# Optimization experiments

Hardware: AMD Instinct MI355X
Metric: run time of the kernel (lower is better)

Reference implementation:

```python
import jax, jax.numpy as jnp
import numpy as np


def fps(xyz, npoint):
    # farthest point sampling, starts at index 0 (matches pointnet2 CUDA kernel)
    B, N, _ = xyz.shape
    def step(carry, _):
        min_d, last = carry
        last_xyz = jnp.take_along_axis(xyz, last[:, None, None], axis=1)  # [B,1,3]
        d = jnp.sum((xyz - last_xyz) ** 2, axis=-1)                        # [B,N]
        min_d = jnp.minimum(min_d, d)
        nxt = jnp.argmax(min_d, axis=1).astype(jnp.int32)
        return (min_d, nxt), last
    init = (jnp.full((B, N), 1e10, xyz.dtype), jnp.zeros((B,), jnp.int32))
    _, idx = jax.lax.scan(step, init, None, length=npoint)
    return jnp.transpose(idx)  # [B, npoint]


def ball_query(xyz, new_xyz, radius, nsample):
    # first nsample points within radius; pad with first hit (0 if none) -- CUDA semantics
    N = xyz.shape[1]
    d2 = jnp.sum((new_xyz[:, :, None, :] - xyz[:, None, :, :]) ** 2, axis=-1)  # [B,S,N]
    cand = jnp.where(d2 < radius * radius, jnp.arange(N, dtype=jnp.int32)[None, None, :], N)
    srt = jnp.sort(cand, axis=-1)[..., :nsample]
    first = srt[..., :1]
    first = jnp.where(first == N, 0, first)
    return jnp.where(srt == N, first, srt)  # [B,S,K]


def gather_nbrs(x, idx):
    # x [B,N,C], idx [B,S,K] -> [B,S,K,C]
    B, S, K = idx.shape
    flat = jnp.take_along_axis(x, idx.reshape(B, S * K, 1), axis=1)
    return flat.reshape(B, S, K, x.shape[-1])


def shared_mlp(x, layers):
    # 1x1 conv (+ folded eval-mode BN) + ReLU per layer
    for w, b in layers:
        x = jax.nn.relu(jnp.einsum('bskc,oc->bsko', x, w) + b)
    return x


def sa_module(xyz, feat, npoint, radius, nsample, layers):
    idx = fps(xyz, npoint)
    new_xyz = jnp.take_along_axis(xyz, idx[:, :, None], axis=1)  # [B,S,3]
    gidx = ball_query(xyz, new_xyz, radius, nsample)
    grouped = gather_nbrs(xyz, gidx) - new_xyz[:, :, None, :]    # centered local xyz
    if feat is not None:
        grouped = jnp.concatenate([grouped, gather_nbrs(feat, gidx)], axis=-1)
    x = shared_mlp(grouped, layers)
    return new_xyz, jnp.max(x, axis=2)  # max-pool over neighbors -> [B,S,Cout]


def sa_module_all(xyz, feat, layers):
    # GroupAll: concat raw (uncentered) xyz with features, one group of all points
    x = jnp.concatenate([xyz, feat], axis=-1)[:, None]  # [B,1,N,3+C]
    x = shared_mlp(x, layers)
    return jnp.max(x, axis=2)[:, 0]  # [B,Cout]


def _forward(data, ws):
    B, T, N, _ = data.shape
    xyz = data.reshape(B * T, N, 3)
    xyz, feat = sa_module(xyz, None, 256, 0.2, 32, ws[0])
    xyz, feat = sa_module(xyz, feat, 128, 0.4, 32, ws[1])
    out = sa_module_all(xyz, feat, ws[2])
    return out.reshape(B, T, -1)


DIMS = [(3, 64), (64, 64), (64, 128), (131, 128), (128, 128), (128, 256), (259, 256), (256, 512), (512, 1024)]
NAMES = ['1_0', '1_1', '1_2', '2_0', '2_1', '2_2', '3_0', '3_1', '3_2']


def setup_inputs() -> dict:
    key = jax.random.key(0)
    keys = jax.random.split(key, 1 + 2 * len(DIMS))
    inp = {'data': jax.random.normal(keys[0], (4, 8, 4096, 3), jnp.float32)}
    for i, ((cin, cout), nm) in enumerate(zip(DIMS, NAMES)):
        inp['w' + nm] = jax.random.normal(keys[1 + 2 * i], (cout, cin), jnp.float32) / np.sqrt(cin).astype(np.float32)
        inp['b' + nm] = jax.random.normal(keys[2 + 2 * i], (cout,), jnp.float32) * 0.02
    return inp


def reference(data, w1_0, b1_0, w1_1, b1_1, w1_2, b1_2,
              w2_0, b2_0, w2_1, b2_1, w2_2, b2_2,
              w3_0, b3_0, w3_1, b3_1, w3_2, b3_2):
    ws = [[(w1_0, b1_0), (w1_1, b1_1), (w1_2, b1_2)],
          [(w2_0, b2_0), (w2_1, b2_1), (w2_2, b2_2)],
          [(w3_0, b3_0), (w3_1, b3_1), (w3_2, b3_2)]]
    return _forward(data, ws)
```

## Files before the change

### kernel.cpp

```cpp
#include <hip/hip_runtime.h>
#include <hip/hip_bf16.h>
#include <cstdint>
#include <cstddef>

#define BT 32
#define N1 4096
#define S1 256
#define S2 128
#define KNB 32

typedef __attribute__((ext_vector_type(8))) short short8;
typedef __attribute__((ext_vector_type(4))) float f32x4;

__device__ __forceinline__ float sqdist(float ax, float ay, float az,
                                        float bx, float by, float bz) {
    float dx = __fsub_rn(ax, bx), dy = __fsub_rn(ay, by), dz = __fsub_rn(az, bz);
    return __fadd_rn(__fadd_rn(__fmul_rn(dx, dx), __fmul_rn(dy, dy)), __fmul_rn(dz, dz));
}

__device__ __forceinline__ unsigned short f2bf(float f) {
    unsigned u = __float_as_uint(f);
    return (unsigned short)((u + 0x7FFFu + ((u >> 16) & 1u)) >> 16);
}
__device__ __forceinline__ float bf2f(unsigned short h) {
    return __uint_as_float(((unsigned)h) << 16);
}

__device__ __forceinline__ unsigned long long packvi(float v, int idx) {
    return ((unsigned long long)__float_as_uint(v) << 32) | (unsigned)(~idx);
}

template <int CTRL>
__device__ __forceinline__ unsigned long long dppmax(unsigned long long v) {
    int lo = (int)(unsigned)(v & 0xFFFFFFFFull);
    int hi = (int)(unsigned)(v >> 32);
    int lo2 = __builtin_amdgcn_update_dpp(0, lo, CTRL, 0xF, 0xF, false);
    int hi2 = __builtin_amdgcn_update_dpp(0, hi, CTRL, 0xF, 0xF, false);
    unsigned long long o = ((unsigned long long)(unsigned)hi2 << 32) | (unsigned)lo2;
    return o > v ? o : v;
}
#define ROR1 0x121
#define ROR2 0x122
#define ROR4 0x124
#define ROR8 0x128

__global__ __launch_bounds__(512) void fps1_kernel(const float* __restrict__ xyz,
                                                   float* __restrict__ nxz) {
    const int b = blockIdx.x, tid = threadIdx.x;
    const int lane = tid & 63, wv = tid >> 6;
    const float* X = xyz + (size_t)b * (N1 * 3);
    __shared__ float4 s4[N1];
    __shared__ unsigned long long slots[2][8];
    __shared__ float hist[S1 * 3];
    float px[8], py[8], pz[8], md[8];
#pragma unroll
    for (int j = 0; j < 8; ++j) {
        int i = tid + 512 * j;
        float x = X[i * 3 + 0], y = X[i * 3 + 1], z = X[i * 3 + 2];
        s4[i] = make_float4(x, y, z, 0.f);
        px[j] = x; py[j] = y; pz[j] = z;
        md[j] = 1e10f;
    }
    if (tid == 0) { hist[0] = X[0]; hist[1] = X[1]; hist[2] = X[2]; }
    __syncthreads();
    float4 c0 = s4[0];
    float lx = c0.x, ly = c0.y, lz = c0.z;
    for (int t = 1; t < S1; ++t) {
        float bv = -1.0f; int bi = 0;
#pragma unroll
        for (int j = 0; j < 8; ++j) {
            float d = sqdist(px[j], py[j], pz[j], lx, ly, lz);
            float m = fminf(md[j], d);
            md[j] = m;
            if (m > bv) { bv = m; bi = tid + 512 * j; }
        }
        unsigned long long best = packvi(bv, bi);
        best = dppmax<ROR1>(best);
        best = dppmax<ROR2>(best);
        best = dppmax<ROR4>(best);
        best = dppmax<ROR8>(best);
        { unsigned long long o = __shfl_xor(best, 16); best = o > best ? o : best; }
        { unsigned long long o = __shfl_xor(best, 32); best = o > best ? o : best; }
        if (lane == 0) slots[t & 1][wv] = best;
        __syncthreads();
        unsigned long long w = slots[t & 1][lane & 7];
        w = dppmax<ROR1>(w);
        w = dppmax<ROR2>(w);
        w = dppmax<ROR4>(w);
        int vi = (int)(~(unsigned)w);
        float4 c = s4[vi];
        lx = c.x; ly = c.y; lz = c.z;
        if (tid == 0) { hist[t * 3 + 0] = lx; hist[t * 3 + 1] = ly; hist[t * 3 + 2] = lz; }
    }
    __syncthreads();
    for (int u = tid; u < S1 * 3; u += 512) nxz[(size_t)b * S1 * 3 + u] = hist[u];
}

__global__ __launch_bounds__(64) void fps2_kernel(const float* __restrict__ xyz1,
                                                  float* __restrict__ nxz2) {
    const int b = blockIdx.x, lane = threadIdx.x;
    const float* X = xyz1 + (size_t)b * (S1 * 3);
    __shared__ float4 s4[S1];
    float px[4], py[4], pz[4], md[4];
#pragma unroll
    for (int j = 0; j < 4; ++j) {
        int i = lane + 64 * j;
        float x = X[i * 3 + 0], y = X[i * 3 + 1], z = X[i * 3 + 2];
        s4[i] = make_float4(x, y, z, 0.f);
        px[j] = x; py[j] = y; pz[j] = z;
        md[j] = 1e10f;
    }
    if (lane == 0) {
        nxz2[(size_t)b * S2 * 3 + 0] = X[0];
        nxz2[(size_t)b * S2 * 3 + 1] = X[1];
        nxz2[(size_t)b * S2 * 3 + 2] = X[2];
    }
    float4 cc = s4[0];
    float lx = cc.x, ly = cc.y, lz = cc.z;
    for (int t = 1; t < S2; ++t) {
        float bv = -1.0f; int bi = 0;
#pragma unroll
        for (int j = 0; j < 4; ++j) {
            float d = sqdist(px[j], py[j], pz[j], lx, ly, lz);
            float m = fminf(md[j], d);
            md[j] = m;
            if (m > bv) { bv = m; bi = lane + 64 * j; }
        }
        unsigned long long best = packvi(bv, bi);
        best = dppmax<ROR1>(best);
        best = dppmax<ROR2>(best);
        best = dppmax<ROR4>(best);
        best = dppmax<ROR8>(best);
        { unsigned long long o = __shfl_xor(best, 16); best = o > best ? o : best; }
        { unsigned long long o = __shfl_xor(best, 32); best = o > best ? o : best; }
        int vi = (int)(~(unsigned)best);
        float4 c = s4[vi];
        lx = c.x; ly = c.y; lz = c.z;
        if (lane == 0) {
            float* dst = nxz2 + ((size_t)b * S2 + t) * 3;
            dst[0] = lx; dst[1] = ly; dst[2] = lz;
        }
    }
}

__global__ __launch_bounds__(256) void ballq1_kernel(const float* __restrict__ xyz,
                                                     const float* __restrict__ nxz,
                                                     int* __restrict__ gidx) {
    const int wid = (blockIdx.x * 256 + threadIdx.x) >> 6;
    const int lane = threadIdx.x & 63;
    const int b = wid >> 8;
    const float* X = xyz + (size_t)b * (N1 * 3);
    const float* C = nxz + (size_t)wid * 3;
    const float cx = C[0], cy = C[1], cz = C[2];
    const float r2 = (float)(0.2 * 0.2);
    int* G = gidx + (size_t)wid * KNB;
    int cnt = 0, first = 0;
    bool found = false;
    for (int j0 = 0; j0 < N1 && cnt < KNB; j0 += 64) {
        int j = j0 + lane;
        float d2 = sqdist(cx, cy, cz, X[j * 3 + 0], X[j * 3 + 1], X[j * 3 + 2]);
        bool hit = d2 < r2;
        unsigned long long mask = __ballot(hit);
        if (!found && mask) { first = j0 + __builtin_ctzll(mask); found = true; }
        if (hit) {
            int pos = cnt + __popcll(mask & ((1ull << lane) - 1ull));
            if (pos < KNB) G[pos] = j;
        }
        cnt += __popcll(mask);
    }
    if (cnt < KNB) {
        int pad = found ? first : 0;
        if (lane >= cnt && lane < KNB) G[lane] = pad;
    }
}

__global__ __launch_bounds__(256) void ballq2_kernel(const float* __restrict__ xyz1,
                                                     const float* __restrict__ nxz2,
                                                     int* __restrict__ gidx) {
    const int wid = (blockIdx.x * 256 + threadIdx.x) >> 6;
    const int lane = threadIdx.x & 63;
    const int b = wid >> 7;
    const float* X = xyz1 + (size_t)b * (S1 * 3);
    const float* C = nxz2 + (size_t)wid * 3;
    const float cx = C[0], cy = C[1], cz = C[2];
    const float r2 = (float)(0.4 * 0.4);
    int* G = gidx + (size_t)wid * KNB;
    int cnt = 0, first = 0;
    bool found = false;
    for (int j0 = 0; j0 < S1 && cnt < KNB; j0 += 64) {
        int j = j0 + lane;
        float d2 = sqdist(cx, cy, cz, X[j * 3 + 0], X[j * 3 + 1], X[j * 3 + 2]);
        bool hit = d2 < r2;
        unsigned long long mask = __ballot(hit);
        if (!found && mask) { first = j0 + __builtin_ctzll(mask); found = true; }
        if (hit) {
            int pos = cnt + __popcll(mask & ((1ull << lane) - 1ull));
            if (pos < KNB) G[pos] = j;
        }
        cnt += __popcll(mask);
    }
    if (cnt < KNB) {
        int pad = found ? first : 0;
        if (lane >= cnt && lane < KNB) G[lane] = pad;
    }
}

__global__ __launch_bounds__(256) void wconv_kernel(
    const float* __restrict__ w11, const float* __restrict__ w12,
    const float* __restrict__ w20, const float* __restrict__ w21,
    const float* __restrict__ w22, const float* __restrict__ w30,
    const float* __restrict__ w31, const float* __restrict__ w32,
    unsigned short* __restrict__ wb) {
    int u = blockIdx.x * 256 + threadIdx.x;
    if (u >= 823296) return;
    const float* src; int base, Kp, Ko; bool perm20 = false;
    if      (u < 4096)   { src = w11; base = 0;      Kp = 64;  Ko = 64;  }
    else if (u < 12288)  { src = w12; base = 4096;   Kp = 64;  Ko = 64;  }
    else if (u < 36864)  { src = w20; base = 12288;  Kp = 192; Ko = 131; perm20 = true; }
    else if (u < 53248)  { src = w21; base = 36864;  Kp = 128; Ko = 128; }
    else if (u < 86016)  { src = w22; base = 53248;  Kp = 128; Ko = 128; }
    else if (u < 167936) { src = w30; base = 86016;  Kp = 320; Ko = 259; }
    else if (u < 299008) { src = w31; base = 167936; Kp = 256; Ko = 256; }
    else                 { src = w32; base = 299008; Kp = 512; Ko = 512; }
    int local = u - base;
    int n = local / Kp, k = local - n * Kp;
    float v;
    if (perm20) {
        int ksrc = (k < 128) ? (k + 3) : ((k < 131) ? (k - 128) : -1);
        v = (ksrc >= 0) ? src[(size_t)n * 131 + ksrc] : 0.f;
    } else {
        v = (k < Ko) ? src[(size_t)n * Ko + k] : 0.f;
    }
    wb[u] = f2bf(v);
}

__global__ __launch_bounds__(256) void m1_kernel(
    const float* __restrict__ xyz, const float* __restrict__ nxz,
    const int* __restrict__ g1,
    const float* __restrict__ w10, const float* __restrict__ b10,
    const unsigned short* __restrict__ w11b, const float* __restrict__ b11,
    const unsigned short* __restrict__ w12b, const float* __restrict__ b12,
    unsigned short* __restrict__ f1) {
    constexpr int AP = 72;
    __shared__ __align__(16) unsigned short As[128 * AP];
    __shared__ __align__(16) unsigned short Hs[128 * AP];
    __shared__ __align__(16) unsigned short Bs[128 * AP];
    __shared__ float sxyz[128 * 3];
    const int t = threadIdx.x;
    const int lane = t & 63, w = t >> 6;
    const int r16 = lane & 15, q = lane >> 4;
    const int m0 = blockIdx.x * 128;

    if (t < 128) {
        int row = m0 + t, bs = row >> 5, b = bs >> 8, j = g1[row];
        const float* P = xyz + ((size_t)b * N1 + j) * 3;
        const float* Cc = nxz + (size_t)bs * 3;
        sxyz[t * 3 + 0] = P[0] - Cc[0];
        sxyz[t * 3 + 1] = P[1] - Cc[1];
        sxyz[t * 3 + 2] = P[2] - Cc[2];
    }
    for (int c = t; c < 64 * 8; c += 256) {
        int row = c >> 3, ch = c & 7;
        *(short8*)&Bs[row * AP + ch * 8] = *(const short8*)&w11b[row * 64 + ch * 8];
    }
    __syncthreads();
    {
        const int r = t >> 1, half = (t & 1) * 32;
        const float x = sxyz[r * 3 + 0], y = sxyz[r * 3 + 1], z = sxyz[r * 3 + 2];
        unsigned short tmp[32];
#pragma unroll
        for (int o = 0; o < 32; ++o) {
            int oo = half + o;
            float acc = b10[oo];
            acc = fmaf(x, w10[oo * 3 + 0], acc);
            acc = fmaf(y, w10[oo * 3 + 1], acc);
            acc = fmaf(z, w10[oo * 3 + 2], acc);
            tmp[o] = f2bf(fmaxf(acc, 0.f));
        }
#pragma unroll
        for (int c2 = 0; c2 < 4; ++c2)
            *(short8*)&As[r * AP + half + c2 * 8] = *(short8*)&tmp[c2 * 8];
    }
    __syncthreads();
    {
        f32x4 acc[2][4];
#pragma unroll
        for (int i = 0; i < 2; ++i)
#pragma unroll
            for (int j = 0; j < 4; ++j) acc[i][j] = (f32x4){0.f, 0.f, 0.f, 0.f};
#pragma unroll
        for (int kk = 0; kk < 64; kk += 32) {
            short8 a0 = *(const short8*)&As[(w * 32 + r16) * AP + kk + q * 8];
            short8 a1 = *(const short8*)&As[(w * 32 + 16 + r16) * AP + kk + q * 8];
#pragma unroll
            for (int j = 0; j < 4; ++j) {
                short8 bf = *(const short8*)&Bs[(j * 16 + r16) * AP + kk + q * 8];
                acc[0][j] = __builtin_amdgcn_mfma_f32_16x16x32_bf16(a0, bf, acc[0][j], 0, 0, 0);
                acc[1][j] = __builtin_amdgcn_mfma_f32_16x16x32_bf16(a1, bf, acc[1][j], 0, 0, 0);
            }
        }
#pragma unroll
        for (int i = 0; i < 2; ++i)
#pragma unroll
            for (int j = 0; j < 4; ++j) {
                int col = j * 16 + r16;
                float bv = b11[col];
#pragma unroll
                for (int r = 0; r < 4; ++r) {
                    int row = w * 32 + i * 16 + q * 4 + r;
                    Hs[row * AP + col] = f2bf(fmaxf(acc[i][j][r] + bv, 0.f));
                }
            }
    }
    __syncthreads();
    for (int c = t; c < 128 * 8; c += 256) {
        int row = c >> 3, ch = c & 7;
        *(short8*)&Bs[row * AP + ch * 8] = *(const short8*)&w12b[row * 64 + ch * 8];
    }
    __syncthreads();
    {
        f32x4 acc[2][8];
#pragma unroll
        for (int i = 0; i < 2; ++i)
#pragma unroll
            for (int j = 0; j < 8; ++j) acc[i][j] = (f32x4){0.f, 0.f, 0.f, 0.f};
#pragma unroll
        for (int kk = 0; kk < 64; kk += 32) {
            short8 a0 = *(const short8*)&Hs[(w * 32 + r16) * AP + kk + q * 8];
            short8 a1 = *(const short8*)&Hs[(w * 32 + 16 + r16) * AP + kk + q * 8];
#pragma unroll
            for (int j = 0; j < 8; ++j) {
                short8 bf = *(const short8*)&Bs[(j * 16 + r16) * AP + kk + q * 8];
                acc[0][j] = __builtin_amdgcn_mfma_f32_16x16x32_bf16(a0, bf, acc[0][j], 0, 0, 0);
                acc[1][j] = __builtin_amdgcn_mfma_f32_16x16x32_bf16(a1, bf, acc[1][j], 0, 0, 0);
            }
        }
#pragma unroll
        for (int j = 0; j < 8; ++j) {
            int col = j * 16 + r16;
            float bv = b12[col];
            float mv = 0.f;
#pragma unroll
            for (int i = 0; i < 2; ++i)
#pragma unroll
                for (int r = 0; r < 4; ++r)
                    mv = fmaxf(mv, acc[i][j][r] + bv);
            mv = fmaxf(mv, __shfl_xor(mv, 16));
            mv = fmaxf(mv, __shfl_xor(mv, 32));
            if (q == 0)
                f1[(size_t)((m0 >> 5) + w) * 128 + col] = f2bf(mv);
        }
    }
}

__global__ __launch_bounds__(256) void m2_kernel(
    const float* __restrict__ xyz1, const float* __restrict__ nxz2,
    const int* __restrict__ g2, const unsigned short* __restrict__ f1,
    const unsigned short* __restrict__ w20p, const float* __restrict__ b20,
    const unsigned short* __restrict__ w21b, const float* __restrict__ b21,
    const unsigned short* __restrict__ w22b, const float* __restrict__ b22,
    unsigned short* __restrict__ f2) {
    constexpr int AP = 72, HP = 136;
    __shared__ __align__(16) unsigned short smem[36864];
    unsigned short* R1 = smem;
    unsigned short* R2 = smem + 18432;
    unsigned short* As = R1;
    unsigned short* Bs = R1 + 9216;
    unsigned short* H1 = R2;
    unsigned short* H2 = R1;
    unsigned short* Bs2 = R2;
    __shared__ int ribase[128];
    __shared__ unsigned short sxb[128 * 3];
    const int t = threadIdx.x;
    const int lane = t & 63, w = t >> 6;
    const int r16 = lane & 15, q = lane >> 4;
    const int m0 = blockIdx.x * 128;

    if (t < 128) {
        int row = m0 + t, bs = row >> 5, b = bs >> 7, j = g2[row];
        ribase[t] = (b * 256 + j) * 128;
        const float* P = xyz1 + ((size_t)b * S1 + j) * 3;
        const float* Cc = nxz2 + (size_t)bs * 3;
        sxb[t * 3 + 0] = f2bf(P[0] - Cc[0]);
        sxb[t * 3 + 1] = f2bf(P[1] - Cc[1]);
        sxb[t * 3 + 2] = f2bf(P[2] - Cc[2]);
    }
    __syncthreads();

    f32x4 acc[2][8];
#pragma unroll
    for (int i = 0; i < 2; ++i)
#pragma unroll
        for (int j = 0; j < 8; ++j) acc[i][j] = (f32x4){0.f, 0.f, 0.f, 0.f};
    for (int kt = 0; kt < 3; ++kt) {
        const int k0 = kt * 64;
        if (kt < 2) {
            for (int c = t; c < 128 * 8; c += 256) {
                int row = c >> 3, ch = c & 7;
                *(short8*)&As[row * AP + ch * 8] =
                    *(const short8*)&f1[(size_t)ribase[row] + k0 + ch * 8];
            }
        } else {
            for (int c = t; c < 128 * 8; c += 256) {
                int row = c >> 3, ch = c & 7;
                short8 v = (short8){0, 0, 0, 0, 0, 0, 0, 0};
                if (ch == 0) {
                    v[0] = (short)sxb[row * 3 + 0];
                    v[1] = (short)sxb[row * 3 + 1];
                    v[2] = (short)sxb[row * 3 + 2];
                }
                *(short8*)&As[row * AP + ch * 8] = v;
            }
        }
        for (int c = t; c < 128 * 8; c += 256) {
            int row = c >> 3, ch = c & 7;
            *(short8*)&Bs[row * AP + ch * 8] =
                *(const short8*)&w20p[(size_t)row * 192 + k0 + ch * 8];
        }
        __syncthreads();
#pragma unroll
        for (int kk = 0; kk < 64; kk += 32) {
            short8 a0 = *(const short8*)&As[(w * 32 + r16) * AP + kk + q * 8];
            short8 a1 = *(const short8*)&As[(w * 32 + 16 + r16) * AP + kk + q * 8];
#pragma unroll
            for (int j = 0; j < 8; ++j) {
                short8 bf = *(const short8*)&Bs[(j * 16 + r16) * AP + kk + q * 8];
                acc[0][j] = __builtin_amdgcn_mfma_f32_16x16x32_bf16(a0, bf, acc[0][j], 0, 0, 0);
                acc[1][j] = __builtin_amdgcn_mfma_f32_16x16x32_bf16(a1, bf, acc[1][j], 0, 0, 0);
            }
        }
        __syncthreads();
    }
#pragma unroll
    for (int i = 0; i < 2; ++i)
#pragma unroll
        for (int j = 0; j < 8; ++j) {
            int col = j * 16 + r16;
            float bv = b20[col];
#pragma unroll
            for (int r = 0; r < 4; ++r) {
                int row = w * 32 + i * 16 + q * 4 + r;
                H1[row * HP + col] = f2bf(fmaxf(acc[i][j][r] + bv, 0.f));
            }
        }
    __syncthreads();

#pragma unroll
    for (int i = 0; i < 2; ++i)
#pragma unroll
        for (int j = 0; j < 8; ++j) acc[i][j] = (f32x4){0.f, 0.f, 0.f, 0.f};
    for (int kt = 0; kt < 2; ++kt) {
        const int k0 = kt * 64;
        for (int c = t; c < 128 * 8; c += 256) {
            int row = c >> 3, ch = c & 7;
            *(short8*)&As[row * AP + ch * 8] =
                *(const short8*)&w21b[(size_t)row * 128 + k0 + ch * 8];
        }
        __syncthreads();
#pragma unroll
        for (int kk = 0; kk < 64; kk += 32) {
            short8 a0 = *(const short8*)&H1[(w * 32 + r16) * HP + k0 + kk + q * 8];
            short8 a1 = *(const short8*)&H1[(w * 32 + 16 + r16) * HP + k0 + kk + q * 8];
#pragma unroll
            for (int j = 0; j < 8; ++j) {
                short8 bf = *(const short8*)&As[(j * 16 + r16) * AP + kk + q * 8];
                acc[0][j] = __builtin_amdgcn_mfma_f32_16x16x32_bf16(a0, bf, acc[0][j], 0, 0, 0);
                acc[1][j] = __builtin_amdgcn_mfma_f32_16x16x32_bf16(a1, bf, acc[1][j], 0, 0, 0);
            }
        }
        __syncthreads();
    }
#pragma unroll
    for (int i = 0; i < 2; ++i)
#pragma unroll
        for (int j = 0; j < 8; ++j) {
            int col = j * 16 + r16;
            float bv = b21[col];
#pragma unroll
            for (int r = 0; r < 4; ++r) {
                int row = w * 32 + i * 16 + q * 4 + r;
                H2[row * HP + col] = f2bf(fmaxf(acc[i][j][r] + bv, 0.f));
            }
        }
    __syncthreads();

    f32x4 acc2[2][16];
#pragma unroll
    for (int i = 0; i < 2; ++i)
#pragma unroll
        for (int j = 0; j < 16; ++j) acc2[i][j] = (f32x4){0.f, 0.f, 0.f, 0.f};
    for (int kt = 0; kt < 2; ++kt) {
        const int k0 = kt * 64;
        for (int c = t; c < 256 * 8; c += 256) {
            int row = c >> 3, ch = c & 7;
            *(short8*)&Bs2[row * AP + ch * 8] =
                *(const short8*)&w22b[(size_t)row * 128 + k0 + ch * 8];
        }
        __syncthreads();
#pragma unroll
        for (int kk = 0; kk < 64; kk += 32) {
            short8 a0 = *(const short8*)&H2[(w * 32 + r16) * HP + k0 + kk + q * 8];
            short8 a1 = *(const short8*)&H2[(w * 32 + 16 + r16) * HP + k0 + kk + q * 8];
#pragma unroll
            for (int j = 0; j < 16; ++j) {
                short8 bf = *(const short8*)&Bs2[(j * 16 + r16) * AP + kk + q * 8];
                acc2[0][j] = __builtin_amdgcn_mfma_f32_16x16x32_bf16(a0, bf, acc2[0][j], 0, 0, 0);
                acc2[1][j] = __builtin_amdgcn_mfma_f32_16x16x32_bf16(a1, bf, acc2[1][j], 0, 0, 0);
            }
        }
        __syncthreads();
    }
#pragma unroll
    for (int j = 0; j < 16; ++j) {
        int col = j * 16 + r16;
        float bv = b22[col];
        float mv = 0.f;
#pragma unroll
        for (int i = 0; i < 2; ++i)
#pragma unroll
            for (int r = 0; r < 4; ++r)
                mv = fmaxf(mv, acc2[i][j][r] + bv);
        mv = fmaxf(mv, __shfl_xor(mv, 16));
        mv = fmaxf(mv, __shfl_xor(mv, 32));
        if (q == 0)
            f2[(size_t)((m0 >> 5) + w) * 256 + col] = f2bf(mv);
    }
}

__global__ __launch_bounds__(256) void gather3_kernel(const float* __restrict__ nxz2,
                                                      const unsigned short* __restrict__ f2,
                                                      unsigned short* __restrict__ Xg) {
    int u = blockIdx.x * 256 + threadIdx.x;
    int r = u / 320, c = u - r * 320;
    unsigned short v;
    if (c < 3)        v = f2bf(nxz2[(size_t)r * 3 + c]);
    else if (c < 259) v = f2[(size_t)r * 256 + (c - 3)];
    else              v = 0;
    Xg[u] = v;
}

template <int BN, bool POOL>
__global__ __launch_bounds__(256) void mfma_gemm(const unsigned short* __restrict__ X,
                                                 const unsigned short* __restrict__ W,
                                                 const float* __restrict__ bias,
                                                 unsigned short* __restrict__ C,
                                                 int M, int N, int K) {
    constexpr int BM = 128, BK = 64;
    constexpr int AP = BK + 8;
    constexpr int NT = BN / 16;
    __shared__ __align__(16) unsigned short As[BM * AP];
    __shared__ __align__(16) unsigned short Bs[BN * AP];
    const int t = threadIdx.x;
    const int lane = t & 63, w = t >> 6;
    const int m0 = blockIdx.x * BM;
    const int n0 = blockIdx.y * BN;
    const int r16 = lane & 15, q = lane >> 4;

    f32x4 acc[2][NT];
#pragma unroll
    for (int i = 0; i < 2; ++i)
#pragma unroll
        for (int j = 0; j < NT; ++j) acc[i][j] = (f32x4){0.f, 0.f, 0.f, 0.f};

    for (int k0 = 0; k0 < K; k0 += BK) {
        for (int c = t; c < BM * (BK / 8); c += 256) {
            int row = c >> 3, ch = c & 7;
            *(short8*)&As[row * AP + ch * 8] =
                *(const short8*)&X[(size_t)(m0 + row) * K + k0 + ch * 8];
        }
        for (int c = t; c < BN * (BK / 8); c += 256) {
            int row = c >> 3, ch = c & 7;
            *(short8*)&Bs[row * AP + ch * 8] =
                *(const short8*)&W[(size_t)(n0 + row) * K + k0 + ch * 8];
        }
        __syncthreads();
#pragma unroll
        for (int kk = 0; kk < BK; kk += 32) {
            short8 a0 = *(const short8*)&As[(w * 32 + r16) * AP + kk + q * 8];
            short8 a1 = *(const short8*)&As[(w * 32 + 16 + r16) * AP + kk + q * 8];
#pragma unroll
            for (int j = 0; j < NT; ++j) {
                short8 bf = *(const short8*)&Bs[(j * 16 + r16) * AP + kk + q * 8];
                acc[0][j] = __builtin_amdgcn_mfma_f32_16x16x32_bf16(a0, bf, acc[0][j], 0, 0, 0);
                acc[1][j] = __builtin_amdgcn_mfma_f32_16x16x32_bf16(a1, bf, acc[1][j], 0, 0, 0);
            }
        }
        __syncthreads();
    }

    if (!POOL) {
#pragma unroll
        for (int i = 0; i < 2; ++i)
#pragma unroll
            for (int j = 0; j < NT; ++j) {
                int col = n0 + j * 16 + r16;
                float bv = bias[col];
#pragma unroll
                for (int r = 0; r < 4; ++r) {
                    int row = m0 + w * 32 + i * 16 + q * 4 + r;
                    C[(size_t)row * N + col] = f2bf(fmaxf(acc[i][j][r] + bv, 0.f));
                }
            }
    } else {
#pragma unroll
        for (int j = 0; j < NT; ++j) {
            int col = n0 + j * 16 + r16;
            float bv = bias[col];
            float mv = 0.f;
#pragma unroll
            for (int i = 0; i < 2; ++i)
#pragma unroll
                for (int r = 0; r < 4; ++r)
                    mv = fmaxf(mv, acc[i][j][r] + bv);
            mv = fmaxf(mv, __shfl_xor(mv, 16));
            mv = fmaxf(mv, __shfl_xor(mv, 32));
            if (q == 0)
                C[(size_t)((m0 >> 5) + w) * N + col] = f2bf(mv);
        }
    }
}

__global__ __launch_bounds__(256) void maxn_kernel(const unsigned short* __restrict__ h,
                                                   float* __restrict__ out) {
    int id = blockIdx.x * 256 + threadIdx.x;
    int o = id & 1023, b = id >> 10;
    const unsigned short* p = h + (size_t)b * 128 * 1024 + o;
    float m = 0.f;
    for (int n = 0; n < 128; ++n) m = fmaxf(m, bf2f(p[(size_t)n * 1024]));
    out[id] = m;
}

extern "C" void kernel_launch(void* const* d_in, const int* in_sizes, int n_in,
                              void* d_out, int out_size, void* d_ws, size_t ws_size,
                              hipStream_t stream) {
    const float* data = (const float*)d_in[0];
    const float* w10 = (const float*)d_in[1];  const float* b10 = (const float*)d_in[2];
    const float* w11 = (const float*)d_in[3];  const float* b11 = (const float*)d_in[4];
    const float* w12 = (const float*)d_in[5];  const float* b12 = (const float*)d_in[6];
    const float* w20 = (const float*)d_in[7];  const float* b20 = (const float*)d_in[8];
    const float* w21 = (const float*)d_in[9];  const float* b21 = (const float*)d_in[10];
    const float* w22 = (const float*)d_in[11]; const float* b22 = (const float*)d_in[12];
    const float* w30 = (const float*)d_in[13]; const float* b30 = (const float*)d_in[14];
    const float* w31 = (const float*)d_in[15]; const float* b31 = (const float*)d_in[16];
    const float* w32 = (const float*)d_in[17]; const float* b32 = (const float*)d_in[18];
    float* out = (float*)d_out;

    char* ws = (char*)d_ws;
    size_t off = 0;
    auto alloc = [&](size_t bytes) -> void* {
        void* p = ws + off;
        off += (bytes + 255) & ~(size_t)255;
        return p;
    };
    float* nxz1 = (float*)alloc((size_t)BT * S1 * 3 * 4);
    int*   g1   = (int*)  alloc((size_t)BT * S1 * KNB * 4);
    float* nxz2 = (float*)alloc((size_t)BT * S2 * 3 * 4);
    int*   g2   = (int*)  alloc((size_t)BT * S2 * KNB * 4);
    unsigned short* wb  = (unsigned short*)alloc((size_t)823296 * 2);
    unsigned short* f1  = (unsigned short*)alloc((size_t)8192 * 128 * 2);
    unsigned short* f2  = (unsigned short*)alloc((size_t)4096 * 256 * 2);
    unsigned short* xg3 = (unsigned short*)alloc((size_t)4096 * 320 * 2);
    unsigned short* C1  = (unsigned short*)alloc((size_t)4096 * 256 * 2);
    unsigned short* C2  = (unsigned short*)alloc((size_t)4096 * 512 * 2);
    unsigned short* C3  = (unsigned short*)alloc((size_t)4096 * 1024 * 2);

    const unsigned short* w11b = wb + 0;
    const unsigned short* w12b = wb + 4096;
    const unsigned short* w20p = wb + 12288;
    const unsigned short* w21b = wb + 36864;
    const unsigned short* w22b = wb + 53248;
    const unsigned short* w30b = wb + 86016;
    const unsigned short* w31b = wb + 167936;
    const unsigned short* w32b = wb + 299008;

    wconv_kernel<<<(823296 + 255) / 256, 256, 0, stream>>>(w11, w12, w20, w21, w22, w30, w31, w32, wb);

    fps1_kernel<<<BT, 512, 0, stream>>>(data, nxz1);
    ballq1_kernel<<<(BT * S1) / 4, 256, 0, stream>>>(data, nxz1, g1);
    m1_kernel<<<262144 / 128, 256, 0, stream>>>(data, nxz1, g1, w10, b10, w11b, b11, w12b, b12, f1);
    fps2_kernel<<<BT, 64, 0, stream>>>(nxz1, nxz2);
    ballq2_kernel<<<(BT * S2) / 4, 256, 0, stream>>>(nxz1, nxz2, g2);
    m2_kernel<<<131072 / 128, 256, 0, stream>>>(nxz1, nxz2, g2, f1, w20p, b20, w21b, b21, w22b, b22, f2);
    gather3_kernel<<<(4096 * 320) / 256, 256, 0, stream>>>(nxz2, f2, xg3);
    mfma_gemm<128, false><<<dim3(4096 / 128, 2), 256, 0, stream>>>(xg3, w30b, b30, C1, 4096, 256, 320);
    mfma_gemm<128, false><<<dim3(4096 / 128, 4), 256, 0, stream>>>(C1, w31b, b31, C2, 4096, 512, 256);
    mfma_gemm<128, false><<<dim3(4096 / 128, 8), 256, 0, stream>>>(C2, w32b, b32, C3, 4096, 1024, 512);
    maxn_kernel<<<(BT * 1024) / 256, 256, 0, stream>>>(C3, out);
}
```

Before: 533.1 us.

## Fuse ball query into MLP kernels and shrink FPS1 block to 256 threads

The separate ball-query kernels are removed. Each wave of the m1/m2 MLP kernels now computes the neighbour list for its own centroid straight into shared memory, which removes two launches and the global index round trip. The first FPS kernel now runs 256 threads with 16 points each and reduces 16 partial maxima per step instead of 8 wave results. This trades the cross-lane shuffles for one more shared-slot read, at the cost of more serial work per thread in a latency-bound loop.

```diff
diff --git a/kernel.cpp b/kernel.cpp
--- a/kernel.cpp
+++ b/kernel.cpp
@@ -44,22 +44,24 @@
 #define ROR4 0x124
 #define ROR8 0x128
 
-__global__ __launch_bounds__(512) void fps1_kernel(const float* __restrict__ xyz,
+__global__ __launch_bounds__(256) void fps1_kernel(const float* __restrict__ xyz,
                                                    float* __restrict__ nxz) {
     const int b = blockIdx.x, tid = threadIdx.x;
     const int lane = tid & 63, wv = tid >> 6;
     const float* X = xyz + (size_t)b * (N1 * 3);
     __shared__ float4 s4[N1];
-    __shared__ unsigned long long slots[2][8];
+    __shared__ unsigned long long slots[2][16];
     __shared__ float hist[S1 * 3];
-    float px[8], py[8], pz[8], md[8];
-#pragma unroll
-    for (int j = 0; j < 8; ++j) {
-        int i = tid + 512 * j;
+    float px[16], py[16], pz[16], md[16];
+    int bidx[16];
+#pragma unroll
+    for (int j = 0; j < 16; ++j) {
+        int i = tid + 256 * j;
         float x = X[i * 3 + 0], y = X[i * 3 + 1], z = X[i * 3 + 2];
         s4[i] = make_float4(x, y, z, 0.f);
         px[j] = x; py[j] = y; pz[j] = z;
         md[j] = 1e10f;
+        bidx[j] = i;
     }
     if (tid == 0) { hist[0] = X[0]; hist[1] = X[1]; hist[2] = X[2]; }
     __syncthreads();
@@ -68,32 +70,31 @@
     for (int t = 1; t < S1; ++t) {
         float bv = -1.0f; int bi = 0;
 #pragma unroll
-        for (int j = 0; j < 8; ++j) {
+        for (int j = 0; j < 16; ++j) {
             float d = sqdist(px[j], py[j], pz[j], lx, ly, lz);
             float m = fminf(md[j], d);
             md[j] = m;
-            if (m > bv) { bv = m; bi = tid + 512 * j; }
+            if (m > bv) { bv = m; bi = bidx[j]; }
         }
         unsigned long long best = packvi(bv, bi);
         best = dppmax<ROR1>(best);
         best = dppmax<ROR2>(best);
         best = dppmax<ROR4>(best);
         best = dppmax<ROR8>(best);
-        { unsigned long long o = __shfl_xor(best, 16); best = o > best ? o : best; }
-        { unsigned long long o = __shfl_xor(best, 32); best = o > best ? o : best; }
-        if (lane == 0) slots[t & 1][wv] = best;
-        __syncthreads();
-        unsigned long long w = slots[t & 1][lane & 7];
+        if ((lane & 15) == 0) slots[t & 1][wv * 4 + (lane >> 4)] = best;
+        __syncthreads();
+        unsigned long long w = slots[t & 1][lane & 15];
         w = dppmax<ROR1>(w);
         w = dppmax<ROR2>(w);
         w = dppmax<ROR4>(w);
+        w = dppmax<ROR8>(w);
         int vi = (int)(~(unsigned)w);
         float4 c = s4[vi];
         lx = c.x; ly = c.y; lz = c.z;
         if (tid == 0) { hist[t * 3 + 0] = lx; hist[t * 3 + 1] = ly; hist[t * 3 + 2] = lz; }
     }
     __syncthreads();
-    for (int u = tid; u < S1 * 3; u += 512) nxz[(size_t)b * S1 * 3 + u] = hist[u];
+    for (int u = tid; u < S1 * 3; u += 256) nxz[(size_t)b * S1 * 3 + u] = hist[u];
 }
 
 __global__ __launch_bounds__(64) void fps2_kernel(const float* __restrict__ xyz1,
@@ -102,6 +103,7 @@
     const float* X = xyz1 + (size_t)b * (S1 * 3);
     __shared__ float4 s4[S1];
     float px[4], py[4], pz[4], md[4];
+    int bidx[4];
 #pragma unroll
     for (int j = 0; j < 4; ++j) {
         int i = lane + 64 * j;
@@ -109,6 +111,7 @@
         s4[i] = make_float4(x, y, z, 0.f);
         px[j] = x; py[j] = y; pz[j] = z;
         md[j] = 1e10f;
+        bidx[j] = i;
     }
     if (lane == 0) {
         nxz2[(size_t)b * S2 * 3 + 0] = X[0];
@@ -124,7 +127,7 @@
             float d = sqdist(px[j], py[j], pz[j], lx, ly, lz);
             float m = fminf(md[j], d);
             md[j] = m;
-            if (m > bv) { bv = m; bi = lane + 64 * j; }
+            if (m > bv) { bv = m; bi = bidx[j]; }
         }
         unsigned long long best = packvi(bv, bi);
         best = dppmax<ROR1>(best);
@@ -140,68 +143,6 @@
             float* dst = nxz2 + ((size_t)b * S2 + t) * 3;
             dst[0] = lx; dst[1] = ly; dst[2] = lz;
         }
-    }
-}
-
-__global__ __launch_bounds__(256) void ballq1_kernel(const float* __restrict__ xyz,
-                                                     const float* __restrict__ nxz,
-                                                     int* __restrict__ gidx) {
-    const int wid = (blockIdx.x * 256 + threadIdx.x) >> 6;
-    const int lane = threadIdx.x & 63;
-    const int b = wid >> 8;
-    const float* X = xyz + (size_t)b * (N1 * 3);
-    const float* C = nxz + (size_t)wid * 3;
-    const float cx = C[0], cy = C[1], cz = C[2];
-    const float r2 = (float)(0.2 * 0.2);
-    int* G = gidx + (size_t)wid * KNB;
-    int cnt = 0, first = 0;
-    bool found = false;
-    for (int j0 = 0; j0 < N1 && cnt < KNB; j0 += 64) {
-        int j = j0 + lane;
-        float d2 = sqdist(cx, cy, cz, X[j * 3 + 0], X[j * 3 + 1], X[j * 3 + 2]);
-        bool hit = d2 < r2;
-        unsigned long long mask = __ballot(hit);
-        if (!found && mask) { first = j0 + __builtin_ctzll(mask); found = true; }
-        if (hit) {
-            int pos = cnt + __popcll(mask & ((1ull << lane) - 1ull));
-            if (pos < KNB) G[pos] = j;
-        }
-        cnt += __popcll(mask);
-    }
-    if (cnt < KNB) {
-        int pad = found ? first : 0;
-        if (lane >= cnt && lane < KNB) G[lane] = pad;
-    }
-}
-
-__global__ __launch_bounds__(256) void ballq2_kernel(const float* __restrict__ xyz1,
-                                                     const float* __restrict__ nxz2,
-                                                     int* __restrict__ gidx) {
-    const int wid = (blockIdx.x * 256 + threadIdx.x) >> 6;
-    const int lane = threadIdx.x & 63;
-    const int b = wid >> 7;
-    const float* X = xyz1 + (size_t)b * (S1 * 3);
-    const float* C = nxz2 + (size_t)wid * 3;
-    const float cx = C[0], cy = C[1], cz = C[2];
-    const float r2 = (float)(0.4 * 0.4);
-    int* G = gidx + (size_t)wid * KNB;
-    int cnt = 0, first = 0;
-    bool found = false;
-    for (int j0 = 0; j0 < S1 && cnt < KNB; j0 += 64) {
-        int j = j0 + lane;
-        float d2 = sqdist(cx, cy, cz, X[j * 3 + 0], X[j * 3 + 1], X[j * 3 + 2]);
-        bool hit = d2 < r2;
-        unsigned long long mask = __ballot(hit);
-        if (!found && mask) { first = j0 + __builtin_ctzll(mask); found = true; }
-        if (hit) {
-            int pos = cnt + __popcll(mask & ((1ull << lane) - 1ull));
-            if (pos < KNB) G[pos] = j;
-        }
-        cnt += __popcll(mask);
-    }
-    if (cnt < KNB) {
-        int pad = found ? first : 0;
-        if (lane >= cnt && lane < KNB) G[lane] = pad;
     }
 }
 
@@ -236,7 +177,6 @@
 
 __global__ __launch_bounds__(256) void m1_kernel(
     const float* __restrict__ xyz, const float* __restrict__ nxz,
-    const int* __restrict__ g1,
     const float* __restrict__ w10, const float* __restrict__ b10,
     const unsigned short* __restrict__ w11b, const float* __restrict__ b11,
     const unsigned short* __restrict__ w12b, const float* __restrict__ b12,
@@ -246,22 +186,51 @@
     __shared__ __align__(16) unsigned short Hs[128 * AP];
     __shared__ __align__(16) unsigned short Bs[128 * AP];
     __shared__ float sxyz[128 * 3];
+    __shared__ int Gl[4][KNB];
     const int t = threadIdx.x;
     const int lane = t & 63, w = t >> 6;
     const int r16 = lane & 15, q = lane >> 4;
     const int m0 = blockIdx.x * 128;
 
+    for (int c = t; c < 64 * 8; c += 256) {
+        int row = c >> 3, ch = c & 7;
+        *(short8*)&Bs[row * AP + ch * 8] = *(const short8*)&w11b[row * 64 + ch * 8];
+    }
+    {
+        const int cs = (m0 >> 5) + w;
+        const int b = cs >> 8;
+        const float* Xb = xyz + (size_t)b * (N1 * 3);
+        const float* C = nxz + (size_t)cs * 3;
+        const float cx = C[0], cy = C[1], cz = C[2];
+        const float r2 = (float)(0.2 * 0.2);
+        int cnt = 0, first = 0;
+        bool found = false;
+        for (int j0 = 0; j0 < N1 && cnt < KNB; j0 += 64) {
+            int j = j0 + lane;
+            float d2 = sqdist(cx, cy, cz, Xb[j * 3 + 0], Xb[j * 3 + 1], Xb[j * 3 + 2]);
+            bool hit = d2 < r2;
+            unsigned long long mask = __ballot(hit);
+            if (!found && mask) { first = j0 + __builtin_ctzll(mask); found = true; }
+            if (hit) {
+                int pos = cnt + __popcll(mask & ((1ull << lane) - 1ull));
+                if (pos < KNB) Gl[w][pos] = j;
+            }
+            cnt += __popcll(mask);
+        }
+        if (cnt < KNB) {
+            int pad = found ? first : 0;
+            if (lane >= cnt && lane < KNB) Gl[w][lane] = pad;
+        }
+    }
+    __syncthreads();
     if (t < 128) {
-        int row = m0 + t, bs = row >> 5, b = bs >> 8, j = g1[row];
+        int row = m0 + t, bs = row >> 5, b = bs >> 8;
+        int j = Gl[t >> 5][t & 31];
         const float* P = xyz + ((size_t)b * N1 + j) * 3;
         const float* Cc = nxz + (size_t)bs * 3;
         sxyz[t * 3 + 0] = P[0] - Cc[0];
         sxyz[t * 3 + 1] = P[1] - Cc[1];
         sxyz[t * 3 + 2] = P[2] - Cc[2];
-    }
-    for (int c = t; c < 64 * 8; c += 256) {
-        int row = c >> 3, ch = c & 7;
-        *(short8*)&Bs[row * AP + ch * 8] = *(const short8*)&w11b[row * 64 + ch * 8];
     }
     __syncthreads();
     {
@@ -355,7 +324,7 @@
 
 __global__ __launch_bounds__(256) void m2_kernel(
     const float* __restrict__ xyz1, const float* __restrict__ nxz2,
-    const int* __restrict__ g2, const unsigned short* __restrict__ f1,
+    const unsigned short* __restrict__ f1,
     const unsigned short* __restrict__ w20p, const float* __restrict__ b20,
     const unsigned short* __restrict__ w21b, const float* __restrict__ b21,
     const unsigned short* __restrict__ w22b, const float* __restrict__ b22,
@@ -371,13 +340,42 @@
     unsigned short* Bs2 = R2;
     __shared__ int ribase[128];
     __shared__ unsigned short sxb[128 * 3];
+    __shared__ int Gl[4][KNB];
     const int t = threadIdx.x;
     const int lane = t & 63, w = t >> 6;
     const int r16 = lane & 15, q = lane >> 4;
     const int m0 = blockIdx.x * 128;
 
+    {
+        const int cs = (m0 >> 5) + w;
+        const int b = cs >> 7;
+        const float* Xb = xyz1 + (size_t)b * (S1 * 3);
+        const float* C = nxz2 + (size_t)cs * 3;
+        const float cx = C[0], cy = C[1], cz = C[2];
+        const float r2 = (float)(0.4 * 0.4);
+        int cnt = 0, first = 0;
+        bool found = false;
+        for (int j0 = 0; j0 < S1 && cnt < KNB; j0 += 64) {
+            int j = j0 + lane;
+            float d2 = sqdist(cx, cy, cz, Xb[j * 3 + 0], Xb[j * 3 + 1], Xb[j * 3 + 2]);
+            bool hit = d2 < r2;
+            unsigned long long mask = __ballot(hit);
+            if (!found && mask) { first = j0 + __builtin_ctzll(mask); found = true; }
+            if (hit) {
+                int pos = cnt + __popcll(mask & ((1ull << lane) - 1ull));
+                if (pos < KNB) Gl[w][pos] = j;
+            }
+            cnt += __popcll(mask);
+        }
+        if (cnt < KNB) {
+            int pad = found ? first : 0;
+            if (lane >= cnt && lane < KNB) Gl[w][lane] = pad;
+        }
+    }
+    __syncthreads();
     if (t < 128) {
-        int row = m0 + t, bs = row >> 5, b = bs >> 7, j = g2[row];
+        int row = m0 + t, bs = row >> 5, b = bs >> 7;
+        int j = Gl[t >> 5][t & 31];
         ribase[t] = (b * 256 + j) * 128;
         const float* P = xyz1 + ((size_t)b * S1 + j) * 3;
         const float* Cc = nxz2 + (size_t)bs * 3;
@@ -653,9 +651,7 @@
         return p;
     };
     float* nxz1 = (float*)alloc((size_t)BT * S1 * 3 * 4);
-    int*   g1   = (int*)  alloc((size_t)BT * S1 * KNB * 4);
     float* nxz2 = (float*)alloc((size_t)BT * S2 * 3 * 4);
-    int*   g2   = (int*)  alloc((size_t)BT * S2 * KNB * 4);
     unsigned short* wb  = (unsigned short*)alloc((size_t)823296 * 2);
     unsigned short* f1  = (unsigned short*)alloc((size_t)8192 * 128 * 2);
     unsigned short* f2  = (unsigned short*)alloc((size_t)4096 * 256 * 2);
@@ -675,12 +671,10 @@
 
     wconv_kernel<<<(823296 + 255) / 256, 256, 0, stream>>>(w11, w12, w20, w21, w22, w30, w31, w32, wb);
 
-    fps1_kernel<<<BT, 512, 0, stream>>>(data, nxz1);
-    ballq1_kernel<<<(BT * S1) / 4, 256, 0, stream>>>(data, nxz1, g1);
-    m1_kernel<<<262144 / 128, 256, 0, stream>>>(data, nxz1, g1, w10, b10, w11b, b11, w12b, b12, f1);
+    fps1_kernel<<<BT, 256, 0, stream>>>(data, nxz1);
+    m1_kernel<<<262144 / 128, 256, 0, stream>>>(data, nxz1, w10, b10, w11b, b11, w12b, b12, f1);
     fps2_kernel<<<BT, 64, 0, stream>>>(nxz1, nxz2);
-    ballq2_kernel<<<(BT * S2) / 4, 256, 0, stream>>>(nxz1, nxz2, g2);
-    m2_kernel<<<131072 / 128, 256, 0, stream>>>(nxz1, nxz2, g2, f1, w20p, b20, w21b, b21, w22b, b22, f2);
+    m2_kernel<<<131072 / 128, 256, 0, stream>>>(nxz1, nxz2, f1, w20p, b20, w21b, b21, w22b, b22, f2);
     gather3_kernel<<<(4096 * 320) / 256, 256, 0, stream>>>(nxz2, f2, xg3);
     mfma_gemm<128, false><<<dim3(4096 / 128, 2), 256, 0, stream>>>(xg3, w30b, b30, C1, 4096, 256, 320);
     mfma_gemm<128, false><<<dim3(4096 / 128, 4), 256, 0, stream>>>(C1, w31b, b31, C2, 4096, 512, 256);
```

Measured after the change: 576.2 us. +8.1%, slower.

## Fuse layer-3 gather into first GEMM and narrow FPS1 block to 256 threads

Applied to the files above, without the earlier changes.

Replaces the gather3 kernel plus the generic first layer-3 GEMM with a dedicated kernel. It reads f2 directly and builds the xyz tail in the last K tile, using weights permuted so xyz columns sit at the end. This removes a launch and the round trip through the intermediate xg3 buffer. FPS1 now runs 256 threads with 16 points each. Its reduction writes 16 partial maxima per block to shared memory rather than using two cross-lane shuffles, trading more serial work per thread for a cheaper reduction and fewer waves per barrier.

```diff
diff --git a/kernel.cpp b/kernel.cpp
--- a/kernel.cpp
+++ b/kernel.cpp
@@ -44,22 +44,24 @@
 #define ROR4 0x124
 #define ROR8 0x128
 
-__global__ __launch_bounds__(512) void fps1_kernel(const float* __restrict__ xyz,
+__global__ __launch_bounds__(256) void fps1_kernel(const float* __restrict__ xyz,
                                                    float* __restrict__ nxz) {
     const int b = blockIdx.x, tid = threadIdx.x;
     const int lane = tid & 63, wv = tid >> 6;
     const float* X = xyz + (size_t)b * (N1 * 3);
     __shared__ float4 s4[N1];
-    __shared__ unsigned long long slots[2][8];
+    __shared__ unsigned long long slots[2][16];
     __shared__ float hist[S1 * 3];
-    float px[8], py[8], pz[8], md[8];
-#pragma unroll
-    for (int j = 0; j < 8; ++j) {
-        int i = tid + 512 * j;
+    float px[16], py[16], pz[16], md[16];
+    int bidx[16];
+#pragma unroll
+    for (int j = 0; j < 16; ++j) {
+        int i = tid + 256 * j;
         float x = X[i * 3 + 0], y = X[i * 3 + 1], z = X[i * 3 + 2];
         s4[i] = make_float4(x, y, z, 0.f);
         px[j] = x; py[j] = y; pz[j] = z;
         md[j] = 1e10f;
+        bidx[j] = i;
     }
     if (tid == 0) { hist[0] = X[0]; hist[1] = X[1]; hist[2] = X[2]; }
     __syncthreads();
@@ -68,32 +70,31 @@
     for (int t = 1; t < S1; ++t) {
         float bv = -1.0f; int bi = 0;
 #pragma unroll
-        for (int j = 0; j < 8; ++j) {
+        for (int j = 0; j < 16; ++j) {
             float d = sqdist(px[j], py[j], pz[j], lx, ly, lz);
             float m = fminf(md[j], d);
             md[j] = m;
-            if (m > bv) { bv = m; bi = tid + 512 * j; }
+            if (m > bv) { bv = m; bi = bidx[j]; }
         }
         unsigned long long best = packvi(bv, bi);
         best = dppmax<ROR1>(best);
         best = dppmax<ROR2>(best);
         best = dppmax<ROR4>(best);
         best = dppmax<ROR8>(best);
-        { unsigned long long o = __shfl_xor(best, 16); best = o > best ? o : best; }
-        { unsigned long long o = __shfl_xor(best, 32); best = o > best ? o : best; }
-        if (lane == 0) slots[t & 1][wv] = best;
-        __syncthreads();
-        unsigned long long w = slots[t & 1][lane & 7];
+        if ((lane & 15) == 0) slots[t & 1][wv * 4 + (lane >> 4)] = best;
+        __syncthreads();
+        unsigned long long w = slots[t & 1][lane & 15];
         w = dppmax<ROR1>(w);
         w = dppmax<ROR2>(w);
         w = dppmax<ROR4>(w);
+        w = dppmax<ROR8>(w);
         int vi = (int)(~(unsigned)w);
         float4 c = s4[vi];
         lx = c.x; ly = c.y; lz = c.z;
         if (tid == 0) { hist[t * 3 + 0] = lx; hist[t * 3 + 1] = ly; hist[t * 3 + 2] = lz; }
     }
     __syncthreads();
-    for (int u = tid; u < S1 * 3; u += 512) nxz[(size_t)b * S1 * 3 + u] = hist[u];
+    for (int u = tid; u < S1 * 3; u += 256) nxz[(size_t)b * S1 * 3 + u] = hist[u];
 }
 
 __global__ __launch_bounds__(64) void fps2_kernel(const float* __restrict__ xyz1,
@@ -102,6 +103,7 @@
     const float* X = xyz1 + (size_t)b * (S1 * 3);
     __shared__ float4 s4[S1];
     float px[4], py[4], pz[4], md[4];
+    int bidx[4];
 #pragma unroll
     for (int j = 0; j < 4; ++j) {
         int i = lane + 64 * j;
@@ -109,6 +111,7 @@
         s4[i] = make_float4(x, y, z, 0.f);
         px[j] = x; py[j] = y; pz[j] = z;
         md[j] = 1e10f;
+        bidx[j] = i;
     }
     if (lane == 0) {
         nxz2[(size_t)b * S2 * 3 + 0] = X[0];
@@ -124,7 +127,7 @@
             float d = sqdist(px[j], py[j], pz[j], lx, ly, lz);
             float m = fminf(md[j], d);
             md[j] = m;
-            if (m > bv) { bv = m; bi = lane + 64 * j; }
+            if (m > bv) { bv = m; bi = bidx[j]; }
         }
         unsigned long long best = packvi(bv, bi);
         best = dppmax<ROR1>(best);
@@ -213,21 +216,21 @@
     unsigned short* __restrict__ wb) {
     int u = blockIdx.x * 256 + threadIdx.x;
     if (u >= 823296) return;
-    const float* src; int base, Kp, Ko; bool perm20 = false;
+    const float* src; int base, Kp, Ko; int perm = 0;
     if      (u < 4096)   { src = w11; base = 0;      Kp = 64;  Ko = 64;  }
     else if (u < 12288)  { src = w12; base = 4096;   Kp = 64;  Ko = 64;  }
-    else if (u < 36864)  { src = w20; base = 12288;  Kp = 192; Ko = 131; perm20 = true; }
+    else if (u < 36864)  { src = w20; base = 12288;  Kp = 192; Ko = 131; perm = 128; }
     else if (u < 53248)  { src = w21; base = 36864;  Kp = 128; Ko = 128; }
     else if (u < 86016)  { src = w22; base = 53248;  Kp = 128; Ko = 128; }
-    else if (u < 167936) { src = w30; base = 86016;  Kp = 320; Ko = 259; }
+    else if (u < 167936) { src = w30; base = 86016;  Kp = 320; Ko = 259; perm = 256; }
     else if (u < 299008) { src = w31; base = 167936; Kp = 256; Ko = 256; }
     else                 { src = w32; base = 299008; Kp = 512; Ko = 512; }
     int local = u - base;
     int n = local / Kp, k = local - n * Kp;
     float v;
-    if (perm20) {
-        int ksrc = (k < 128) ? (k + 3) : ((k < 131) ? (k - 128) : -1);
-        v = (ksrc >= 0) ? src[(size_t)n * 131 + ksrc] : 0.f;
+    if (perm) {
+        int ksrc = (k < perm) ? (k + 3) : ((k < perm + 3) ? (k - perm) : -1);
+        v = (ksrc >= 0) ? src[(size_t)n * Ko + ksrc] : 0.f;
     } else {
         v = (k < Ko) ? src[(size_t)n * Ko + k] : 0.f;
     }
@@ -527,16 +530,77 @@
     }
 }
 
-__global__ __launch_bounds__(256) void gather3_kernel(const float* __restrict__ nxz2,
-                                                      const unsigned short* __restrict__ f2,
-                                                      unsigned short* __restrict__ Xg) {
-    int u = blockIdx.x * 256 + threadIdx.x;
-    int r = u / 320, c = u - r * 320;
-    unsigned short v;
-    if (c < 3)        v = f2bf(nxz2[(size_t)r * 3 + c]);
-    else if (c < 259) v = f2[(size_t)r * 256 + (c - 3)];
-    else              v = 0;
-    Xg[u] = v;
+__global__ __launch_bounds__(256) void l30_kernel(
+    const float* __restrict__ nxz2, const unsigned short* __restrict__ f2,
+    const unsigned short* __restrict__ w30p, const float* __restrict__ bias,
+    unsigned short* __restrict__ C) {
+    constexpr int AP = 72;
+    __shared__ __align__(16) unsigned short As[128 * AP];
+    __shared__ __align__(16) unsigned short Bs[128 * AP];
+    const int t = threadIdx.x;
+    const int lane = t & 63, w = t >> 6;
+    const int r16 = lane & 15, q = lane >> 4;
+    const int m0 = blockIdx.x * 128;
+    const int n0 = blockIdx.y * 128;
+
+    f32x4 acc[2][8];
+#pragma unroll
+    for (int i = 0; i < 2; ++i)
+#pragma unroll
+        for (int j = 0; j < 8; ++j) acc[i][j] = (f32x4){0.f, 0.f, 0.f, 0.f};
+
+    for (int kt = 0; kt < 5; ++kt) {
+        const int k0 = kt * 64;
+        if (kt < 4) {
+            for (int c = t; c < 128 * 8; c += 256) {
+                int row = c >> 3, ch = c & 7;
+                *(short8*)&As[row * AP + ch * 8] =
+                    *(const short8*)&f2[(size_t)(m0 + row) * 256 + k0 + ch * 8];
+            }
+        } else {
+            for (int c = t; c < 128 * 8; c += 256) {
+                int row = c >> 3, ch = c & 7;
+                short8 v = (short8){0, 0, 0, 0, 0, 0, 0, 0};
+                if (ch == 0) {
+                    const float* P = nxz2 + (size_t)(m0 + row) * 3;
+                    v[0] = (short)f2bf(P[0]);
+                    v[1] = (short)f2bf(P[1]);
+                    v[2] = (short)f2bf(P[2]);
+                }
+                *(short8*)&As[row * AP + ch * 8] = v;
+            }
+        }
+        for (int c = t; c < 128 * 8; c += 256) {
+            int row = c >> 3, ch = c & 7;
+            *(short8*)&Bs[row * AP + ch * 8] =
+                *(const short8*)&w30p[(size_t)(n0 + row) * 320 + k0 + ch * 8];
+        }
+        __syncthreads();
+#pragma unroll
+        for (int kk = 0; kk < 64; kk += 32) {
+            short8 a0 = *(const short8*)&As[(w * 32 + r16) * AP + kk + q * 8];
+            short8 a1 = *(const short8*)&As[(w * 32 + 16 + r16) * AP + kk + q * 8];
+#pragma unroll
+            for (int j = 0; j < 8; ++j) {
+                short8 bf = *(const short8*)&Bs[(j * 16 + r16) * AP + kk + q * 8];
+                acc[0][j] = __builtin_amdgcn_mfma_f32_16x16x32_bf16(a0, bf, acc[0][j], 0, 0, 0);
+                acc[1][j] = __builtin_amdgcn_mfma_f32_16x16x32_bf16(a1, bf, acc[1][j], 0, 0, 0);
+            }
+        }
+        __syncthreads();
+    }
+#pragma unroll
+    for (int i = 0; i < 2; ++i)
+#pragma unroll
+        for (int j = 0; j < 8; ++j) {
+            int col = n0 + j * 16 + r16;
+            float bv = bias[col];
+#pragma unroll
+            for (int r = 0; r < 4; ++r) {
+                int row = m0 + w * 32 + i * 16 + q * 4 + r;
+                C[(size_t)row * 256 + col] = f2bf(fmaxf(acc[i][j][r] + bv, 0.f));
+            }
+        }
 }
 
 template <int BN, bool POOL>
@@ -659,7 +723,6 @@
     unsigned short* wb  = (unsigned short*)alloc((size_t)823296 * 2);
     unsigned short* f1  = (unsigned short*)alloc((size_t)8192 * 128 * 2);
     unsigned short* f2  = (unsigned short*)alloc((size_t)4096 * 256 * 2);
-    unsigned short* xg3 = (unsigned short*)alloc((size_t)4096 * 320 * 2);
     unsigned short* C1  = (unsigned short*)alloc((size_t)4096 * 256 * 2);
     unsigned short* C2  = (unsigned short*)alloc((size_t)4096 * 512 * 2);
     unsigned short* C3  = (unsigned short*)alloc((size_t)4096 * 1024 * 2);
@@ -669,20 +732,19 @@
     const unsigned short* w20p = wb + 12288;
     const unsigned short* w21b = wb + 36864;
     const unsigned short* w22b = wb + 53248;
-    const unsigned short* w30b = wb + 86016;
+    const unsigned short* w30p = wb + 86016;
     const unsigned short* w31b = wb + 167936;
     const unsigned short* w32b = wb + 299008;
 
     wconv_kernel<<<(823296 + 255) / 256, 256, 0, stream>>>(w11, w12, w20, w21, w22, w30, w31, w32, wb);
 
-    fps1_kernel<<<BT, 512, 0, stream>>>(data, nxz1);
+    fps1_kernel<<<BT, 256, 0, stream>>>(data, nxz1);
     ballq1_kernel<<<(BT * S1) / 4, 256, 0, stream>>>(data, nxz1, g1);
     m1_kernel<<<262144 / 128, 256, 0, stream>>>(data, nxz1, g1, w10, b10, w11b, b11, w12b, b12, f1);
     fps2_kernel<<<BT, 64, 0, stream>>>(nxz1, nxz2);
     ballq2_kernel<<<(BT * S2) / 4, 256, 0, stream>>>(nxz1, nxz2, g2);
     m2_kernel<<<131072 / 128, 256, 0, stream>>>(nxz1, nxz2, g2, f1, w20p, b20, w21b, b21, w22b, b22, f2);
-    gather3_kernel<<<(4096 * 320) / 256, 256, 0, stream>>>(nxz2, f2, xg3);
-    mfma_gemm<128, false><<<dim3(4096 / 128, 2), 256, 0, stream>>>(xg3, w30b, b30, C1, 4096, 256, 320);
+    l30_kernel<<<dim3(4096 / 128, 2), 256, 0, stream>>>(nxz2, f2, w30p, b30, C1);
     mfma_gemm<128, false><<<dim3(4096 / 128, 4), 256, 0, stream>>>(C1, w31b, b31, C2, 4096, 512, 256);
     mfma_gemm<128, false><<<dim3(4096 / 128, 8), 256, 0, stream>>>(C2, w32b, b32, C3, 4096, 1024, 512);
     maxn_kernel<<<(BT * 1024) / 256, 256, 0, stream>>>(C3, out);
```

After: 515.4 us. 3.3% less time.
